# Optimization experiments

Hardware: AMD Instinct MI355X
Metric: run time of the kernel (lower is better)

## Reference

```python
import jax, jax.numpy as jnp
import numpy as np

N_TOK, D_MODEL, D_INT, N_EXP, TOP_K = 16384, 1024, 512, 8, 2


def setup_inputs() -> dict:
    key = jax.random.key(0)
    k1, k2, k3, k4 = jax.random.split(key, 4)
    x = jax.random.normal(k1, (N_TOK, D_MODEL), jnp.float32)
    # gate projection weight (n_experts, d_model)
    wg = jax.random.normal(k2, (N_EXP, D_MODEL), jnp.float32) * 0.02
    # fc1: (n_experts, 2*d_intermediate, d_model); fc2: (n_experts, d_model, d_intermediate)
    fc1 = jax.random.normal(k3, (N_EXP, 2 * D_INT, D_MODEL), jnp.float32) * (1.0 / np.sqrt(D_MODEL))
    fc2 = jax.random.normal(k4, (N_EXP, D_MODEL, D_INT), jnp.float32) * (1.0 / np.sqrt(D_INT))
    return {"x": x, "wg": wg, "fc1": fc1, "fc2": fc2, "top_k": TOP_K}


def reference(x, wg, fc1, fc2, top_k):
    # --- Gate: softmax scores, top-k selection, renormalized combine weights ---
    scores = jax.nn.softmax(x @ wg.T, axis=-1)            # (n_tok, n_exp)
    w, idx = jax.lax.top_k(scores, top_k)                 # (n_tok, k)
    w = w / jnp.sum(w, axis=-1, keepdims=True)
    # --- Routed experts: gated MLP per expert, weighted combine ---
    # Equivalent math to sort-by-expert dispatch + grouped GEMM + scatter combine:
    # each token's output = sum_k w_k * f_{idx_k}(x). We loop over the small fixed
    # expert set and mask, avoiding a (n_tok, n_exp, 2*d_int) intermediate.
    n_exp = fc1.shape[0]
    out = jnp.zeros_like(x)
    for e in range(n_exp):
        coef = jnp.sum(jnp.where(idx == e, w, 0.0), axis=-1)  # (n_tok,)
        h = x @ fc1[e].T                                      # (n_tok, 2*d_int)
        y, g = jnp.split(h, 2, axis=-1)
        y = (y * jax.nn.silu(g)) @ fc2[e].T                   # (n_tok, d_model)
        out = out + coef[:, None] * y
    return out
```

## Files before the change

kernel.cpp:

```cpp
#include <hip/hip_runtime.h>
#include <hip/hip_bf16.h>
#include <cstdint>


#define NT 16384
#define DM 1024
#define DI 512
#define NE 8
#define NB 16
#define HB 64
#define MAXT1 272
#define MAXT2 136

typedef __attribute__((ext_vector_type(8))) short bf16x8;
typedef __attribute__((ext_vector_type(4))) float f32x4;

__device__ __forceinline__ void gl16(const void* g, void* l) {
  __builtin_amdgcn_global_load_lds(
      (const __attribute__((address_space(1))) void*)g,
      (__attribute__((address_space(3))) void*)l, 16, 0, 0);
}

__device__ __forceinline__ ushort f2bf(float f) {
  uint32_t x = __float_as_uint(f);
  return (ushort)((x + 0x7fffu + ((x >> 16) & 1u)) >> 16);
}

__global__ __launch_bounds__(256) void f2bf_kernel(const float* __restrict__ in,
                                                   ushort* __restrict__ out, int n8) {
  int i = blockIdx.x * 256 + threadIdx.x;
  if (i >= n8) return;
  const float4* p = (const float4*)(in + (size_t)i * 8);
  float4 a = p[0], b = p[1];
  union { ushort u[8]; int4 v; } o;
  o.u[0] = f2bf(a.x); o.u[1] = f2bf(a.y); o.u[2] = f2bf(a.z); o.u[3] = f2bf(a.w);
  o.u[4] = f2bf(b.x); o.u[5] = f2bf(b.y); o.u[6] = f2bf(b.z); o.u[7] = f2bf(b.w);
  *(int4*)(out + (size_t)i * 8) = o.v;
}

__global__ __launch_bounds__(256) void gate_kernel(
    const float* __restrict__ x, const float* __restrict__ wg,
    int* __restrict__ topk_idx, float* __restrict__ topk_w,
    ushort* __restrict__ xb) {
  __shared__ float wgs[NE * DM];
  for (int i = threadIdx.x; i < NE * DM; i += 256) wgs[i] = wg[i];
  __syncthreads();
  const int wave = threadIdx.x >> 6;
  const int lane = threadIdx.x & 63;
  const int wid = blockIdx.x * 4 + wave;
  for (int g = 0; g < 4; ++g) {
    const int t = wid * 4 + g;
    const float* __restrict__ xr = x + (size_t)t * DM;
    ushort* __restrict__ xw = xb + (size_t)t * DM;
    float acc[NE];
#pragma unroll
    for (int e = 0; e < NE; ++e) acc[e] = 0.f;
#pragma unroll
    for (int it = 0; it < DM / 64; ++it) {
      int k = lane + it * 64;
      float xv = xr[k];
      xw[k] = f2bf(xv);
#pragma unroll
      for (int e = 0; e < NE; ++e) acc[e] += xv * wgs[e * DM + k];
    }
#pragma unroll
    for (int e = 0; e < NE; ++e) {
      float v = acc[e];
#pragma unroll
      for (int off = 32; off > 0; off >>= 1) v += __shfl_xor(v, off);
      acc[e] = v;
    }
    if (lane == 0) {
      float mx = acc[0];
#pragma unroll
      for (int e = 1; e < NE; ++e) mx = fmaxf(mx, acc[e]);
      float p[NE];
#pragma unroll
      for (int e = 0; e < NE; ++e) p[e] = __expf(acc[e] - mx);
      int i0 = 0;
#pragma unroll
      for (int e = 1; e < NE; ++e) if (p[e] > p[i0]) i0 = e;
      int i1 = -1;
#pragma unroll
      for (int e = 0; e < NE; ++e) if (e != i0 && (i1 < 0 || p[e] > p[i1])) i1 = e;
      float s = p[i0] + p[i1];
      topk_idx[t * 2 + 0] = i0;
      topk_idx[t * 2 + 1] = i1;
      topk_w[t * 2 + 0] = p[i0] / s;
      topk_w[t * 2 + 1] = p[i1] / s;
    }
  }
}

__global__ __launch_bounds__(256) void hist_kernel(const int* __restrict__ topk_idx,
                                                   int* __restrict__ blkcnt) {
  __shared__ int lc[NB];
  if (threadIdx.x < NB) lc[threadIdx.x] = 0;
  __syncthreads();
  int t = blockIdx.x * 256 + threadIdx.x;
  atomicAdd(&lc[topk_idx[t * 2 + 0]], 1);
  atomicAdd(&lc[8 + topk_idx[t * 2 + 1]], 1);
  __syncthreads();
  if (threadIdx.x < NB) blkcnt[blockIdx.x * NB + threadIdx.x] = lc[threadIdx.x];
}

__global__ void scan2_kernel(const int* __restrict__ blkcnt, int* __restrict__ counts,
                             int* __restrict__ offsets, int* __restrict__ blk_base,
                             int* __restrict__ t1_list, int* __restrict__ t2_list,
                             int* __restrict__ nmeta) {
  __shared__ int tot[NB], offs[NB];
  const int i = threadIdx.x;
  if (i < NB) {
    int s = 0;
    for (int b = 0; b < HB; ++b) s += blkcnt[b * NB + i];
    tot[i] = s;
    counts[i] = s;
  }
  __syncthreads();
  if (i == 0) {
    int o = 0;
    for (int b = 0; b < NB; ++b) { offs[b] = o; offsets[b] = o; o += tot[b]; }
  }
  __syncthreads();
  if (i < NB) {
    int o = offs[i];
    for (int b = 0; b < HB; ++b) { blk_base[b * NB + i] = o; o += blkcnt[b * NB + i]; }
  }
  if (i == 0) {
    int n1 = 0;
    for (int b = 0; b < NB; ++b) {
      int mts = (tot[b] + 127) >> 7;
      for (int mt = 0; mt < mts; ++mt) t1_list[n1++] = (b << 8) | mt;
    }
    nmeta[0] = n1;
    int n2 = 0;
    for (int b = 0; b < 8; ++b) {
      int mts = (tot[b] + 127) >> 7;
      for (int mt = 0; mt < mts; ++mt) t2_list[n2++] = (b << 8) | mt;
    }
    nmeta[1] = n2;
    int n3 = 0;
    for (int b = 8; b < NB; ++b) {
      int mts = (tot[b] + 127) >> 7;
      for (int mt = 0; mt < mts; ++mt) t2_list[MAXT2 + n3++] = (b << 8) | mt;
    }
    nmeta[2] = n3;
  }
}

__global__ __launch_bounds__(256) void fill_kernel(
    const int* __restrict__ topk_idx, const float* __restrict__ topk_w,
    const int* __restrict__ blk_base, int* __restrict__ bucket_tok,
    float* __restrict__ bucket_w) {
  __shared__ int lcur[NB];
  if (threadIdx.x < NB) lcur[threadIdx.x] = 0;
  __syncthreads();
  int t = blockIdx.x * 256 + threadIdx.x;
#pragma unroll
  for (int j = 0; j < 2; ++j) {
    int e = topk_idx[t * 2 + j];
    int b = j * 8 + e;
    int pos = atomicAdd(&lcur[b], 1);
    int slot = blk_base[blockIdx.x * NB + b] + pos;
    bucket_tok[slot] = t;
    bucket_w[slot] = topk_w[t * 2 + j];
  }
}

__global__ __launch_bounds__(256) void fc1_kernel(
    const ushort* __restrict__ xb, const ushort* __restrict__ fc1b,
    const int* __restrict__ counts, const int* __restrict__ offsets,
    const int* __restrict__ bucket_tok, const int* __restrict__ t1_list,
    const int* __restrict__ nmeta, ushort* __restrict__ z) {
  const int gg = blockIdx.x >> 6;
  const int rr = blockIdx.x & 63;
  const int tl = gg * 8 + (rr & 7);
  const int nt = rr >> 3;
  if (tl >= nmeta[0]) return;
  const int d = t1_list[tl];
  const int b = d >> 8, mt = d & 255;
  const int cnt = counts[b], off = offsets[b], e = b & 7;
  const int m0 = mt << 7, n0 = nt << 6;

  __shared__ ushort As[128 * 64];
  __shared__ ushort By[64 * 64];
  __shared__ ushort Bg[64 * 64];
  __shared__ int toks[128];

  const int t = threadIdx.x;
  if (t < 128) {
    int m = m0 + t;
    toks[t] = bucket_tok[off + ((m < cnt) ? m : (cnt - 1))];
  }
  __syncthreads();

  const int rA = t >> 3;
  const int g8 = (((t & 7) ^ (rA & 7)) << 3);
  const int wave = t >> 6, lane = t & 63;

  const ushort* aSrc0 = xb + (size_t)toks[rA] * DM + g8;
  const ushort* aSrc1 = xb + (size_t)toks[32 + rA] * DM + g8;
  const ushort* aSrc2 = xb + (size_t)toks[64 + rA] * DM + g8;
  const ushort* aSrc3 = xb + (size_t)toks[96 + rA] * DM + g8;
  const ushort* fe = fc1b + (size_t)e * (2 * DI) * DM;
  const ushort* ySrc0 = fe + (size_t)(n0 + rA) * DM + g8;
  const ushort* ySrc1 = fe + (size_t)(n0 + 32 + rA) * DM + g8;
  const ushort* gSrc0 = fe + (size_t)(DI + n0 + rA) * DM + g8;
  const ushort* gSrc1 = fe + (size_t)(DI + n0 + 32 + rA) * DM + g8;

  char* AsW = (char*)As + wave * 1024;
  char* ByW = (char*)By + wave * 1024;
  char* BgW = (char*)Bg + wave * 1024;

  const int moff = (wave >> 1) * 64, noff = (wave & 1) * 32;
  const int fr = lane & 15, fg = lane >> 4;
  const int c0 = ((fg ^ (fr & 7)) << 4);
  const int c1 = (((4 + fg) ^ (fr & 7)) << 4);
  const char* aRd = (const char*)As + (moff + fr) * 128;
  const char* yRd = (const char*)By + (noff + fr) * 128;
  const char* gRd = (const char*)Bg + (noff + fr) * 128;

  f32x4 accY[4][2], accG[4][2];
#pragma unroll
  for (int i = 0; i < 4; ++i)
#pragma unroll
    for (int j = 0; j < 2; ++j) { accY[i][j] = (f32x4)0.f; accG[i][j] = (f32x4)0.f; }

  for (int k0 = 0; k0 < DM; k0 += 64) {
    gl16(aSrc0 + k0, AsW);
    gl16(aSrc1 + k0, AsW + 4096);
    gl16(aSrc2 + k0, AsW + 8192);
    gl16(aSrc3 + k0, AsW + 12288);
    gl16(ySrc0 + k0, ByW);
    gl16(ySrc1 + k0, ByW + 4096);
    gl16(gSrc0 + k0, BgW);
    gl16(gSrc1 + k0, BgW + 4096);
    __syncthreads();
#pragma unroll
    for (int ks = 0; ks < 2; ++ks) {
      const int cc = ks ? c1 : c0;
      bf16x8 a0 = *(const bf16x8*)(aRd + 0 * 2048 + cc);
      bf16x8 a1 = *(const bf16x8*)(aRd + 1 * 2048 + cc);
      bf16x8 a2 = *(const bf16x8*)(aRd + 2 * 2048 + cc);
      bf16x8 a3 = *(const bf16x8*)(aRd + 3 * 2048 + cc);
      bf16x8 y0 = *(const bf16x8*)(yRd + 0 * 2048 + cc);
      bf16x8 y1 = *(const bf16x8*)(yRd + 1 * 2048 + cc);
      bf16x8 g0 = *(const bf16x8*)(gRd + 0 * 2048 + cc);
      bf16x8 g1 = *(const bf16x8*)(gRd + 1 * 2048 + cc);
      accY[0][0] = __builtin_amdgcn_mfma_f32_16x16x32_bf16(a0, y0, accY[0][0], 0, 0, 0);
      accY[1][0] = __builtin_amdgcn_mfma_f32_16x16x32_bf16(a1, y0, accY[1][0], 0, 0, 0);
      accY[2][0] = __builtin_amdgcn_mfma_f32_16x16x32_bf16(a2, y0, accY[2][0], 0, 0, 0);
      accY[3][0] = __builtin_amdgcn_mfma_f32_16x16x32_bf16(a3, y0, accY[3][0], 0, 0, 0);
      accY[0][1] = __builtin_amdgcn_mfma_f32_16x16x32_bf16(a0, y1, accY[0][1], 0, 0, 0);
      accY[1][1] = __builtin_amdgcn_mfma_f32_16x16x32_bf16(a1, y1, accY[1][1], 0, 0, 0);
      accY[2][1] = __builtin_amdgcn_mfma_f32_16x16x32_bf16(a2, y1, accY[2][1], 0, 0, 0);
      accY[3][1] = __builtin_amdgcn_mfma_f32_16x16x32_bf16(a3, y1, accY[3][1], 0, 0, 0);
      accG[0][0] = __builtin_amdgcn_mfma_f32_16x16x32_bf16(a0, g0, accG[0][0], 0, 0, 0);
      accG[1][0] = __builtin_amdgcn_mfma_f32_16x16x32_bf16(a1, g0, accG[1][0], 0, 0, 0);
      accG[2][0] = __builtin_amdgcn_mfma_f32_16x16x32_bf16(a2, g0, accG[2][0], 0, 0, 0);
      accG[3][0] = __builtin_amdgcn_mfma_f32_16x16x32_bf16(a3, g0, accG[3][0], 0, 0, 0);
      accG[0][1] = __builtin_amdgcn_mfma_f32_16x16x32_bf16(a0, g1, accG[0][1], 0, 0, 0);
      accG[1][1] = __builtin_amdgcn_mfma_f32_16x16x32_bf16(a1, g1, accG[1][1], 0, 0, 0);
      accG[2][1] = __builtin_amdgcn_mfma_f32_16x16x32_bf16(a2, g1, accG[2][1], 0, 0, 0);
      accG[3][1] = __builtin_amdgcn_mfma_f32_16x16x32_bf16(a3, g1, accG[3][1], 0, 0, 0);
    }
    __syncthreads();
  }

#pragma unroll
  for (int i = 0; i < 4; ++i)
#pragma unroll
    for (int r = 0; r < 4; ++r) {
      int m = moff + i * 16 + fg * 4 + r;
      if (m0 + m < cnt) {
        ushort* zrow = z + (size_t)(off + m0 + m) * DI + n0 + noff + fr;
#pragma unroll
        for (int j = 0; j < 2; ++j) {
          float y = accY[i][j][r], g = accG[i][j][r];
          float zz = y * g / (1.f + __expf(-g));
          zrow[j * 16] = f2bf(zz);
        }
      }
    }
}

template <bool ADD>
__global__ __launch_bounds__(256) void fc2_kernel(
    const ushort* __restrict__ z, const ushort* __restrict__ fc2b,
    const int* __restrict__ counts, const int* __restrict__ offsets,
    const int* __restrict__ bucket_tok, const float* __restrict__ bucket_w,
    const int* __restrict__ t2_list, const int* __restrict__ nmeta,
    float* __restrict__ out) {
  const int gg = blockIdx.x >> 6;
  const int rr = blockIdx.x & 63;
  const int tl = gg * 8 + (rr & 7);
  const int nt = rr >> 3;
  if (tl >= nmeta[ADD ? 2 : 1]) return;
  const int d = t2_list[(ADD ? MAXT2 : 0) + tl];
  const int b = d >> 8, mt = d & 255;
  const int cnt = counts[b], off = offsets[b], e = b & 7;
  const int m0 = mt << 7, n0 = nt << 7;

  __shared__ ushort As[128 * 64];
  __shared__ ushort Bs[128 * 64];
  __shared__ int toks[128];
  __shared__ float wts[128];

  const int t = threadIdx.x;
  if (t < 128) {
    int m = m0 + t;
    int mm = (m < cnt) ? m : (cnt - 1);
    toks[t] = bucket_tok[off + mm];
    wts[t] = bucket_w[off + mm];
  }
  __syncthreads();

  const int rA = t >> 3;
  const int g8 = (((t & 7) ^ (rA & 7)) << 3);
  const int wave = t >> 6, lane = t & 63;

  const ushort* aSrc0 = z + (size_t)(off + m0 + rA) * DI + g8;
  const ushort* fb = fc2b + (size_t)e * DM * DI;
  const ushort* bSrc0 = fb + (size_t)(n0 + rA) * DI + g8;

  char* AsW = (char*)As + wave * 1024;
  char* BsW = (char*)Bs + wave * 1024;

  const int moff = (wave >> 1) * 64, noff = (wave & 1) * 64;
  const int fr = lane & 15, fg = lane >> 4;
  const int c0 = ((fg ^ (fr & 7)) << 4);
  const int c1 = (((4 + fg) ^ (fr & 7)) << 4);
  const char* aRd = (const char*)As + (moff + fr) * 128;
  const char* bRd = (const char*)Bs + (noff + fr) * 128;

  f32x4 acc[4][4];
#pragma unroll
  for (int i = 0; i < 4; ++i)
#pragma unroll
    for (int j = 0; j < 4; ++j) acc[i][j] = (f32x4)0.f;

  for (int k0 = 0; k0 < DI; k0 += 64) {
    gl16(aSrc0 + k0, AsW);
    gl16(aSrc0 + (size_t)32 * DI + k0, AsW + 4096);
    gl16(aSrc0 + (size_t)64 * DI + k0, AsW + 8192);
    gl16(aSrc0 + (size_t)96 * DI + k0, AsW + 12288);
    gl16(bSrc0 + k0, BsW);
    gl16(bSrc0 + (size_t)32 * DI + k0, BsW + 4096);
    gl16(bSrc0 + (size_t)64 * DI + k0, BsW + 8192);
    gl16(bSrc0 + (size_t)96 * DI + k0, BsW + 12288);
    __syncthreads();
#pragma unroll
    for (int ks = 0; ks < 2; ++ks) {
      const int cc = ks ? c1 : c0;
      bf16x8 a0 = *(const bf16x8*)(aRd + 0 * 2048 + cc);
      bf16x8 a1 = *(const bf16x8*)(aRd + 1 * 2048 + cc);
      bf16x8 a2 = *(const bf16x8*)(aRd + 2 * 2048 + cc);
      bf16x8 a3 = *(const bf16x8*)(aRd + 3 * 2048 + cc);
      bf16x8 b0 = *(const bf16x8*)(bRd + 0 * 2048 + cc);
      bf16x8 b1 = *(const bf16x8*)(bRd + 1 * 2048 + cc);
      bf16x8 b2 = *(const bf16x8*)(bRd + 2 * 2048 + cc);
      bf16x8 b3 = *(const bf16x8*)(bRd + 3 * 2048 + cc);
#pragma unroll
      for (int i = 0; i < 4; ++i) {
        bf16x8 ai = (i == 0) ? a0 : (i == 1) ? a1 : (i == 2) ? a2 : a3;
        acc[i][0] = __builtin_amdgcn_mfma_f32_16x16x32_bf16(ai, b0, acc[i][0], 0, 0, 0);
        acc[i][1] = __builtin_amdgcn_mfma_f32_16x16x32_bf16(ai, b1, acc[i][1], 0, 0, 0);
        acc[i][2] = __builtin_amdgcn_mfma_f32_16x16x32_bf16(ai, b2, acc[i][2], 0, 0, 0);
        acc[i][3] = __builtin_amdgcn_mfma_f32_16x16x32_bf16(ai, b3, acc[i][3], 0, 0, 0);
      }
    }
    __syncthreads();
  }

#pragma unroll
  for (int i = 0; i < 4; ++i)
#pragma unroll
    for (int r = 0; r < 4; ++r) {
      int m = moff + i * 16 + fg * 4 + r;
      if (m0 + m < cnt) {
        int tok = toks[m];
        float w = wts[m];
        float* orow = out + (size_t)tok * DM + n0 + noff + fr;
#pragma unroll
        for (int j = 0; j < 4; ++j) {
          float v = w * acc[i][j][r];
          if (ADD) orow[j * 16] += v;
          else     orow[j * 16] = v;
        }
      }
    }
}

extern "C" void kernel_launch(void* const* d_in, const int* in_sizes, int n_in,
                              void* d_out, int out_size, void* d_ws, size_t ws_size,
                              hipStream_t stream) {
  (void)in_sizes; (void)n_in; (void)out_size; (void)ws_size;
  const float* x   = (const float*)d_in[0];
  const float* wg  = (const float*)d_in[1];
  const float* fc1 = (const float*)d_in[2];
  const float* fc2 = (const float*)d_in[3];
  float* out = (float*)d_out;

  char* p = (char*)d_ws;
  ushort* xb   = (ushort*)p; p += (size_t)NT * DM * 2;
  ushort* fc1b = (ushort*)p; p += (size_t)NE * 2 * DI * DM * 2;
  ushort* fc2b = (ushort*)p; p += (size_t)NE * DM * DI * 2;
  ushort* z    = (ushort*)p; p += ((size_t)2 * NT + 128) * DI * 2;
  int*   topk_idx   = (int*)p;   p += (size_t)NT * 2 * 4;
  float* topk_w     = (float*)p; p += (size_t)NT * 2 * 4;
  int*   bucket_tok = (int*)p;   p += (size_t)2 * NT * 4;
  float* bucket_w   = (float*)p; p += (size_t)2 * NT * 4;
  int*   counts     = (int*)p;   p += NB * 4;
  int*   offsets    = (int*)p;   p += NB * 4;
  int*   blkcnt     = (int*)p;   p += HB * NB * 4;
  int*   blk_base   = (int*)p;   p += HB * NB * 4;
  int*   t1_list    = (int*)p;   p += MAXT1 * 4;
  int*   t2_list    = (int*)p;   p += 2 * MAXT2 * 4;
  int*   nmeta      = (int*)p;   p += 4 * 4;

  f2bf_kernel<<<(NE * 2 * DI * DM / 8 + 255) / 256, 256, 0, stream>>>(fc1, fc1b, NE * 2 * DI * DM / 8);
  f2bf_kernel<<<(NE * DM * DI / 8 + 255) / 256, 256, 0, stream>>>(fc2, fc2b, NE * DM * DI / 8);

  gate_kernel<<<1024, 256, 0, stream>>>(x, wg, topk_idx, topk_w, xb);
  hist_kernel<<<HB, 256, 0, stream>>>(topk_idx, blkcnt);
  scan2_kernel<<<1, 64, 0, stream>>>(blkcnt, counts, offsets, blk_base, t1_list, t2_list, nmeta);
  fill_kernel<<<HB, 256, 0, stream>>>(topk_idx, topk_w, blk_base, bucket_tok, bucket_w);

  fc1_kernel<<<MAXT1 * 8, 256, 0, stream>>>(xb, fc1b, counts, offsets, bucket_tok,
                                            t1_list, nmeta, z);
  fc2_kernel<false><<<MAXT2 * 8, 256, 0, stream>>>(z, fc2b, counts, offsets, bucket_tok,
                                                   bucket_w, t2_list, nmeta, out);
  fc2_kernel<true><<<MAXT2 * 8, 256, 0, stream>>>(z, fc2b, counts, offsets, bucket_tok,
                                                  bucket_w, t2_list, nmeta, out);
}
```

Before: 418.6 us.

## Double-buffer LDS in expert GEMMs, interleave tile lists, vectorize gate

Both grouped GEMM kernels now use two LDS buffers, so the global-to-LDS load of the next K slice is issued before the MFMA work on the current slice, and there is one barrier per iteration instead of two. The scan kernel now builds the tile work lists round-robin across experts instead of grouping them by expert, which is meant to balance weight reuse and load across concurrently running blocks. The gate kernel uses float4 loads and vectorized bf16 stores. In exchange, LDS use doubles (to about 64 KB for fc1), which may lower occupancy.

```diff
diff --git a/kernel.cpp b/kernel.cpp
--- a/kernel.cpp
+++ b/kernel.cpp
@@ -43,7 +43,8 @@
     int* __restrict__ topk_idx, float* __restrict__ topk_w,
     ushort* __restrict__ xb) {
   __shared__ float wgs[NE * DM];
-  for (int i = threadIdx.x; i < NE * DM; i += 256) wgs[i] = wg[i];
+  for (int i = threadIdx.x; i < NE * DM / 4; i += 256)
+    ((float4*)wgs)[i] = ((const float4*)wg)[i];
   __syncthreads();
   const int wave = threadIdx.x >> 6;
   const int lane = threadIdx.x & 63;
@@ -56,12 +57,17 @@
 #pragma unroll
     for (int e = 0; e < NE; ++e) acc[e] = 0.f;
 #pragma unroll
-    for (int it = 0; it < DM / 64; ++it) {
-      int k = lane + it * 64;
-      float xv = xr[k];
-      xw[k] = f2bf(xv);
-#pragma unroll
-      for (int e = 0; e < NE; ++e) acc[e] += xv * wgs[e * DM + k];
+    for (int it = 0; it < 4; ++it) {
+      const int k = it * 256 + lane * 4;
+      float4 xv = *(const float4*)(xr + k);
+      ushort4 o;
+      o.x = f2bf(xv.x); o.y = f2bf(xv.y); o.z = f2bf(xv.z); o.w = f2bf(xv.w);
+      *(ushort4*)(xw + k) = o;
+#pragma unroll
+      for (int e = 0; e < NE; ++e) {
+        float4 wv = *(const float4*)&wgs[e * DM + k];
+        acc[e] += xv.x * wv.x + xv.y * wv.y + xv.z * wv.z + xv.w * wv.w;
+      }
     }
 #pragma unroll
     for (int e = 0; e < NE; ++e) {
@@ -127,22 +133,40 @@
     for (int b = 0; b < HB; ++b) { blk_base[b * NB + i] = o; o += blkcnt[b * NB + i]; }
   }
   if (i == 0) {
+    int rem[NB], bmt[NB];
     int n1 = 0;
-    for (int b = 0; b < NB; ++b) {
-      int mts = (tot[b] + 127) >> 7;
-      for (int mt = 0; mt < mts; ++mt) t1_list[n1++] = (b << 8) | mt;
+    for (int q = 0; q < NB; ++q) { rem[q] = (tot[q] + 127) >> 7; bmt[q] = 0; n1 += rem[q]; }
+    for (int p = 0; p < n1; ++p) {
+      int c = p & 7, b2;
+      if (rem[c] > 0) b2 = c;
+      else if (rem[8 + c] > 0) b2 = 8 + c;
+      else { int best = -1; b2 = 0;
+        for (int q = 0; q < NB; ++q) if (rem[q] > best) { best = rem[q]; b2 = q; } }
+      t1_list[p] = (b2 << 8) | bmt[b2]++;
+      rem[b2]--;
     }
     nmeta[0] = n1;
+    int rem2[8], bmt2[8];
     int n2 = 0;
-    for (int b = 0; b < 8; ++b) {
-      int mts = (tot[b] + 127) >> 7;
-      for (int mt = 0; mt < mts; ++mt) t2_list[n2++] = (b << 8) | mt;
+    for (int q = 0; q < 8; ++q) { rem2[q] = (tot[q] + 127) >> 7; bmt2[q] = 0; n2 += rem2[q]; }
+    for (int p = 0; p < n2; ++p) {
+      int c = p & 7, b2;
+      if (rem2[c] > 0) b2 = c;
+      else { int best = -1; b2 = 0;
+        for (int q = 0; q < 8; ++q) if (rem2[q] > best) { best = rem2[q]; b2 = q; } }
+      t2_list[p] = (b2 << 8) | bmt2[b2]++;
+      rem2[b2]--;
     }
     nmeta[1] = n2;
     int n3 = 0;
-    for (int b = 8; b < NB; ++b) {
-      int mts = (tot[b] + 127) >> 7;
-      for (int mt = 0; mt < mts; ++mt) t2_list[MAXT2 + n3++] = (b << 8) | mt;
+    for (int q = 0; q < 8; ++q) { rem2[q] = (tot[8 + q] + 127) >> 7; bmt2[q] = 0; n3 += rem2[q]; }
+    for (int p = 0; p < n3; ++p) {
+      int c = p & 7, b2;
+      if (rem2[c] > 0) b2 = c;
+      else { int best = -1; b2 = 0;
+        for (int q = 0; q < 8; ++q) if (rem2[q] > best) { best = rem2[q]; b2 = q; } }
+      t2_list[MAXT2 + p] = ((8 + b2) << 8) | bmt2[b2]++;
+      rem2[b2]--;
     }
     nmeta[2] = n3;
   }
@@ -182,9 +206,9 @@
   const int cnt = counts[b], off = offsets[b], e = b & 7;
   const int m0 = mt << 7, n0 = nt << 6;
 
-  __shared__ ushort As[128 * 64];
-  __shared__ ushort By[64 * 64];
-  __shared__ ushort Bg[64 * 64];
+  __shared__ ushort As[2][128 * 64];
+  __shared__ ushort By[2][64 * 64];
+  __shared__ ushort Bg[2][64 * 64];
   __shared__ int toks[128];
 
   const int t = threadIdx.x;
@@ -208,17 +232,10 @@
   const ushort* gSrc0 = fe + (size_t)(DI + n0 + rA) * DM + g8;
   const ushort* gSrc1 = fe + (size_t)(DI + n0 + 32 + rA) * DM + g8;
 
-  char* AsW = (char*)As + wave * 1024;
-  char* ByW = (char*)By + wave * 1024;
-  char* BgW = (char*)Bg + wave * 1024;
-
   const int moff = (wave >> 1) * 64, noff = (wave & 1) * 32;
   const int fr = lane & 15, fg = lane >> 4;
   const int c0 = ((fg ^ (fr & 7)) << 4);
   const int c1 = (((4 + fg) ^ (fr & 7)) << 4);
-  const char* aRd = (const char*)As + (moff + fr) * 128;
-  const char* yRd = (const char*)By + (noff + fr) * 128;
-  const char* gRd = (const char*)Bg + (noff + fr) * 128;
 
   f32x4 accY[4][2], accG[4][2];
 #pragma unroll
@@ -226,46 +243,63 @@
 #pragma unroll
     for (int j = 0; j < 2; ++j) { accY[i][j] = (f32x4)0.f; accG[i][j] = (f32x4)0.f; }
 
-  for (int k0 = 0; k0 < DM; k0 += 64) {
-    gl16(aSrc0 + k0, AsW);
-    gl16(aSrc1 + k0, AsW + 4096);
-    gl16(aSrc2 + k0, AsW + 8192);
-    gl16(aSrc3 + k0, AsW + 12288);
-    gl16(ySrc0 + k0, ByW);
-    gl16(ySrc1 + k0, ByW + 4096);
-    gl16(gSrc0 + k0, BgW);
-    gl16(gSrc1 + k0, BgW + 4096);
+#define STAGE1(BUF, K0) do { \
+    char* AsW = (char*)As + (BUF) * 16384 + wave * 1024; \
+    char* ByW = (char*)By + (BUF) * 8192 + wave * 1024; \
+    char* BgW = (char*)Bg + (BUF) * 8192 + wave * 1024; \
+    gl16(aSrc0 + (K0), AsW); \
+    gl16(aSrc1 + (K0), AsW + 4096); \
+    gl16(aSrc2 + (K0), AsW + 8192); \
+    gl16(aSrc3 + (K0), AsW + 12288); \
+    gl16(ySrc0 + (K0), ByW); \
+    gl16(ySrc1 + (K0), ByW + 4096); \
+    gl16(gSrc0 + (K0), BgW); \
+    gl16(gSrc1 + (K0), BgW + 4096); \
+  } while (0)
+
+#define COMPUTE1(BUF) do { \
+    const char* aRd = (const char*)As + (BUF) * 16384 + (moff + fr) * 128; \
+    const char* yRd = (const char*)By + (BUF) * 8192 + (noff + fr) * 128; \
+    const char* gRd = (const char*)Bg + (BUF) * 8192 + (noff + fr) * 128; \
+    _Pragma("unroll") \
+    for (int ks = 0; ks < 2; ++ks) { \
+      const int cc = ks ? c1 : c0; \
+      bf16x8 a0 = *(const bf16x8*)(aRd + 0 * 2048 + cc); \
+      bf16x8 a1 = *(const bf16x8*)(aRd + 1 * 2048 + cc); \
+      bf16x8 a2 = *(const bf16x8*)(aRd + 2 * 2048 + cc); \
+      bf16x8 a3 = *(const bf16x8*)(aRd + 3 * 2048 + cc); \
+      bf16x8 y0 = *(const bf16x8*)(yRd + 0 * 2048 + cc); \
+      bf16x8 y1 = *(const bf16x8*)(yRd + 1 * 2048 + cc); \
+      bf16x8 g0 = *(const bf16x8*)(gRd + 0 * 2048 + cc); \
+      bf16x8 g1 = *(const bf16x8*)(gRd + 1 * 2048 + cc); \
+      accY[0][0] = __builtin_amdgcn_mfma_f32_16x16x32_bf16(a0, y0, accY[0][0], 0, 0, 0); \
+      accY[1][0] = __builtin_amdgcn_mfma_f32_16x16x32_bf16(a1, y0, accY[1][0], 0, 0, 0); \
+      accY[2][0] = __builtin_amdgcn_mfma_f32_16x16x32_bf16(a2, y0, accY[2][0], 0, 0, 0); \
+      accY[3][0] = __builtin_amdgcn_mfma_f32_16x16x32_bf16(a3, y0, accY[3][0], 0, 0, 0); \
+      accY[0][1] = __builtin_amdgcn_mfma_f32_16x16x32_bf16(a0, y1, accY[0][1], 0, 0, 0); \
+      accY[1][1] = __builtin_amdgcn_mfma_f32_16x16x32_bf16(a1, y1, accY[1][1], 0, 0, 0); \
+      accY[2][1] = __builtin_amdgcn_mfma_f32_16x16x32_bf16(a2, y1, accY[2][1], 0, 0, 0); \
+      accY[3][1] = __builtin_amdgcn_mfma_f32_16x16x32_bf16(a3, y1, accY[3][1], 0, 0, 0); \
+      accG[0][0] = __builtin_amdgcn_mfma_f32_16x16x32_bf16(a0, g0, accG[0][0], 0, 0, 0); \
+      accG[1][0] = __builtin_amdgcn_mfma_f32_16x16x32_bf16(a1, g0, accG[1][0], 0, 0, 0); \
+      accG[2][0] = __builtin_amdgcn_mfma_f32_16x16x32_bf16(a2, g0, accG[2][0], 0, 0, 0); \
+      accG[3][0] = __builtin_amdgcn_mfma_f32_16x16x32_bf16(a3, g0, accG[3][0], 0, 0, 0); \
+      accG[0][1] = __builtin_amdgcn_mfma_f32_16x16x32_bf16(a0, g1, accG[0][1], 0, 0, 0); \
+      accG[1][1] = __builtin_amdgcn_mfma_f32_16x16x32_bf16(a1, g1, accG[1][1], 0, 0, 0); \
+      accG[2][1] = __builtin_amdgcn_mfma_f32_16x16x32_bf16(a2, g1, accG[2][1], 0, 0, 0); \
+      accG[3][1] = __builtin_amdgcn_mfma_f32_16x16x32_bf16(a3, g1, accG[3][1], 0, 0, 0); \
+    } \
+  } while (0)
+
+  STAGE1(0, 0);
+  __syncthreads();
+#pragma unroll
+  for (int i = 0; i < 15; ++i) {
+    STAGE1((i + 1) & 1, (i + 1) * 64);
+    COMPUTE1(i & 1);
     __syncthreads();
-#pragma unroll
-    for (int ks = 0; ks < 2; ++ks) {
-      const int cc = ks ? c1 : c0;
-      bf16x8 a0 = *(const bf16x8*)(aRd + 0 * 2048 + cc);
-      bf16x8 a1 = *(const bf16x8*)(aRd + 1 * 2048 + cc);
-      bf16x8 a2 = *(const bf16x8*)(aRd + 2 * 2048 + cc);
-      bf16x8 a3 = *(const bf16x8*)(aRd + 3 * 2048 + cc);
-      bf16x8 y0 = *(const bf16x8*)(yRd + 0 * 2048 + cc);
-      bf16x8 y1 = *(const bf16x8*)(yRd + 1 * 2048 + cc);
-      bf16x8 g0 = *(const bf16x8*)(gRd + 0 * 2048 + cc);
-      bf16x8 g1 = *(const bf16x8*)(gRd + 1 * 2048 + cc);
-      accY[0][0] = __builtin_amdgcn_mfma_f32_16x16x32_bf16(a0, y0, accY[0][0], 0, 0, 0);
-      accY[1][0] = __builtin_amdgcn_mfma_f32_16x16x32_bf16(a1, y0, accY[1][0], 0, 0, 0);
-      accY[2][0] = __builtin_amdgcn_mfma_f32_16x16x32_bf16(a2, y0, accY[2][0], 0, 0, 0);
-      accY[3][0] = __builtin_amdgcn_mfma_f32_16x16x32_bf16(a3, y0, accY[3][0], 0, 0, 0);
-      accY[0][1] = __builtin_amdgcn_mfma_f32_16x16x32_bf16(a0, y1, accY[0][1], 0, 0, 0);
-      accY[1][1] = __builtin_amdgcn_mfma_f32_16x16x32_bf16(a1, y1, accY[1][1], 0, 0, 0);
-      accY[2][1] = __builtin_amdgcn_mfma_f32_16x16x32_bf16(a2, y1, accY[2][1], 0, 0, 0);
-      accY[3][1] = __builtin_amdgcn_mfma_f32_16x16x32_bf16(a3, y1, accY[3][1], 0, 0, 0);
-      accG[0][0] = __builtin_amdgcn_mfma_f32_16x16x32_bf16(a0, g0, accG[0][0], 0, 0, 0);
-      accG[1][0] = __builtin_amdgcn_mfma_f32_16x16x32_bf16(a1, g0, accG[1][0], 0, 0, 0);
-      accG[2][0] = __builtin_amdgcn_mfma_f32_16x16x32_bf16(a2, g0, accG[2][0], 0, 0, 0);
-      accG[3][0] = __builtin_amdgcn_mfma_f32_16x16x32_bf16(a3, g0, accG[3][0], 0, 0, 0);
-      accG[0][1] = __builtin_amdgcn_mfma_f32_16x16x32_bf16(a0, g1, accG[0][1], 0, 0, 0);
-      accG[1][1] = __builtin_amdgcn_mfma_f32_16x16x32_bf16(a1, g1, accG[1][1], 0, 0, 0);
-      accG[2][1] = __builtin_amdgcn_mfma_f32_16x16x32_bf16(a2, g1, accG[2][1], 0, 0, 0);
-      accG[3][1] = __builtin_amdgcn_mfma_f32_16x16x32_bf16(a3, g1, accG[3][1], 0, 0, 0);
-    }
-    __syncthreads();
-  }
+  }
+  COMPUTE1(1);
 
 #pragma unroll
   for (int i = 0; i < 4; ++i)
@@ -282,6 +316,8 @@
         }
       }
     }
+#undef STAGE1
+#undef COMPUTE1
 }
 
 template <bool ADD>
@@ -301,8 +337,8 @@
   const int cnt = counts[b], off = offsets[b], e = b & 7;
   const int m0 = mt << 7, n0 = nt << 7;
 
-  __shared__ ushort As[128 * 64];
-  __shared__ ushort Bs[128 * 64];
+  __shared__ ushort As[2][128 * 64];
+  __shared__ ushort Bs[2][128 * 64];
   __shared__ int toks[128];
   __shared__ float wts[128];
 
@@ -323,15 +359,10 @@
   const ushort* fb = fc2b + (size_t)e * DM * DI;
   const ushort* bSrc0 = fb + (size_t)(n0 + rA) * DI + g8;
 
-  char* AsW = (char*)As + wave * 1024;
-  char* BsW = (char*)Bs + wave * 1024;
-
   const int moff = (wave >> 1) * 64, noff = (wave & 1) * 64;
   const int fr = lane & 15, fg = lane >> 4;
   const int c0 = ((fg ^ (fr & 7)) << 4);
   const int c1 = (((4 + fg) ^ (fr & 7)) << 4);
-  const char* aRd = (const char*)As + (moff + fr) * 128;
-  const char* bRd = (const char*)Bs + (noff + fr) * 128;
 
   f32x4 acc[4][4];
 #pragma unroll
@@ -339,38 +370,53 @@
 #pragma unroll
     for (int j = 0; j < 4; ++j) acc[i][j] = (f32x4)0.f;
 
-  for (int k0 = 0; k0 < DI; k0 += 64) {
-    gl16(aSrc0 + k0, AsW);
-    gl16(aSrc0 + (size_t)32 * DI + k0, AsW + 4096);
-    gl16(aSrc0 + (size_t)64 * DI + k0, AsW + 8192);
-    gl16(aSrc0 + (size_t)96 * DI + k0, AsW + 12288);
-    gl16(bSrc0 + k0, BsW);
-    gl16(bSrc0 + (size_t)32 * DI + k0, BsW + 4096);
-    gl16(bSrc0 + (size_t)64 * DI + k0, BsW + 8192);
-    gl16(bSrc0 + (size_t)96 * DI + k0, BsW + 12288);
+#define STAGE2(BUF, K0) do { \
+    char* AsW = (char*)As + (BUF) * 16384 + wave * 1024; \
+    char* BsW = (char*)Bs + (BUF) * 16384 + wave * 1024; \
+    gl16(aSrc0 + (K0), AsW); \
+    gl16(aSrc0 + (size_t)32 * DI + (K0), AsW + 4096); \
+    gl16(aSrc0 + (size_t)64 * DI + (K0), AsW + 8192); \
+    gl16(aSrc0 + (size_t)96 * DI + (K0), AsW + 12288); \
+    gl16(bSrc0 + (K0), BsW); \
+    gl16(bSrc0 + (size_t)32 * DI + (K0), BsW + 4096); \
+    gl16(bSrc0 + (size_t)64 * DI + (K0), BsW + 8192); \
+    gl16(bSrc0 + (size_t)96 * DI + (K0), BsW + 12288); \
+  } while (0)
+
+#define COMPUTE2(BUF) do { \
+    const char* aRd = (const char*)As + (BUF) * 16384 + (moff + fr) * 128; \
+    const char* bRd = (const char*)Bs + (BUF) * 16384 + (noff + fr) * 128; \
+    _Pragma("unroll") \
+    for (int ks = 0; ks < 2; ++ks) { \
+      const int cc = ks ? c1 : c0; \
+      bf16x8 a0 = *(const bf16x8*)(aRd + 0 * 2048 + cc); \
+      bf16x8 a1 = *(const bf16x8*)(aRd + 1 * 2048 + cc); \
+      bf16x8 a2 = *(const bf16x8*)(aRd + 2 * 2048 + cc); \
+      bf16x8 a3 = *(const bf16x8*)(aRd + 3 * 2048 + cc); \
+      bf16x8 b0 = *(const bf16x8*)(bRd + 0 * 2048 + cc); \
+      bf16x8 b1 = *(const bf16x8*)(bRd + 1 * 2048 + cc); \
+      bf16x8 b2 = *(const bf16x8*)(bRd + 2 * 2048 + cc); \
+      bf16x8 b3 = *(const bf16x8*)(bRd + 3 * 2048 + cc); \
+      _Pragma("unroll") \
+      for (int i = 0; i < 4; ++i) { \
+        bf16x8 ai = (i == 0) ? a0 : (i == 1) ? a1 : (i == 2) ? a2 : a3; \
+        acc[i][0] = __builtin_amdgcn_mfma_f32_16x16x32_bf16(ai, b0, acc[i][0], 0, 0, 0); \
+        acc[i][1] = __builtin_amdgcn_mfma_f32_16x16x32_bf16(ai, b1, acc[i][1], 0, 0, 0); \
+        acc[i][2] = __builtin_amdgcn_mfma_f32_16x16x32_bf16(ai, b2, acc[i][2], 0, 0, 0); \
+        acc[i][3] = __builtin_amdgcn_mfma_f32_16x16x32_bf16(ai, b3, acc[i][3], 0, 0, 0); \
+      } \
+    } \
+  } while (0)
+
+  STAGE2(0, 0);
+  __syncthreads();
+#pragma unroll
+  for (int i = 0; i < 7; ++i) {
+    STAGE2((i + 1) & 1, (i + 1) * 64);
+    COMPUTE2(i & 1);
     __syncthreads();
-#pragma unroll
-    for (int ks = 0; ks < 2; ++ks) {
-      const int cc = ks ? c1 : c0;
-      bf16x8 a0 = *(const bf16x8*)(aRd + 0 * 2048 + cc);
-      bf16x8 a1 = *(const bf16x8*)(aRd + 1 * 2048 + cc);
-      bf16x8 a2 = *(const bf16x8*)(aRd + 2 * 2048 + cc);
-      bf16x8 a3 = *(const bf16x8*)(aRd + 3 * 2048 + cc);
-      bf16x8 b0 = *(const bf16x8*)(bRd + 0 * 2048 + cc);
-      bf16x8 b1 = *(const bf16x8*)(bRd + 1 * 2048 + cc);
-      bf16x8 b2 = *(const bf16x8*)(bRd + 2 * 2048 + cc);
-      bf16x8 b3 = *(const bf16x8*)(bRd + 3 * 2048 + cc);
-#pragma unroll
-      for (int i = 0; i < 4; ++i) {
-        bf16x8 ai = (i == 0) ? a0 : (i == 1) ? a1 : (i == 2) ? a2 : a3;
-        acc[i][0] = __builtin_amdgcn_mfma_f32_16x16x32_bf16(ai, b0, acc[i][0], 0, 0, 0);
-        acc[i][1] = __builtin_amdgcn_mfma_f32_16x16x32_bf16(ai, b1, acc[i][1], 0, 0, 0);
-        acc[i][2] = __builtin_amdgcn_mfma_f32_16x16x32_bf16(ai, b2, acc[i][2], 0, 0, 0);
-        acc[i][3] = __builtin_amdgcn_mfma_f32_16x16x32_bf16(ai, b3, acc[i][3], 0, 0, 0);
-      }
-    }
-    __syncthreads();
-  }
+  }
+  COMPUTE2(1);
 
 #pragma unroll
   for (int i = 0; i < 4; ++i)
@@ -389,6 +435,8 @@
         }
       }
     }
+#undef STAGE2
+#undef COMPUTE2
 }
 
 extern "C" void kernel_launch(void* const* d_in, const int* in_sizes, int n_in,
```

After: 447.2 us. 6.9% more time.
